# Kernel optimization log

Measured on AMD Instinct MI355X. Metric: run time of the kernel, lower is better.

The kernel has to match this reference:

```python
import jax, jax.numpy as jnp
import numpy as np

L, B, D = 1024, 24, 512


def setup_inputs() -> dict:
    key = jax.random.key(0)
    ks = jax.random.split(key, 9)
    s = 1.0 / np.sqrt(D)
    return {
        "v": jax.random.normal(ks[0], (L, B, D), dtype=jnp.float32),
        "h0": jax.random.normal(ks[1], (B, D), dtype=jnp.float32),
        "V": jax.random.normal(ks[2], (B, D), dtype=jnp.float32),
        "Wp": jax.random.normal(ks[3], (D, D), dtype=jnp.float32) * s,
        "Wp_": jax.random.normal(ks[4], (D, D), dtype=jnp.float32) * s,
        "w_ih": jax.random.normal(ks[5], (3 * D, D), dtype=jnp.float32) * s,
        "w_hh": jax.random.normal(ks[6], (3 * D, D), dtype=jnp.float32) * s,
        "b_ih": jax.random.normal(ks[7], (3 * D,), dtype=jnp.float32) * s,
        "b_hh": jax.random.normal(ks[8], (3 * D,), dtype=jnp.float32) * s,
    }


def reference(v, h0, V, Wp, Wp_, w_ih, w_hh, b_ih, b_hh):
    # v: [l, b, d]. Precompute both projections once (original wastefully
    # recomputes Wp_(v) per step; the math is identical).
    Wpv_all = jnp.einsum('lbd,hd->lbh', v, Wp)    # per-step query proj
    Wpvp = jnp.einsum('lbd,hd->lbh', v, Wp_)      # shared key proj

    def step(h, wpv_i):
        # additive attention over all l positions
        x = jnp.tanh(wpv_i[None, :, :] + Wpvp)           # [l, b, h]
        s = jnp.einsum('lbh,bh->bl', x, V)               # scores
        a = jax.nn.softmax(s, axis=1)                    # [b, l]
        c = jnp.einsum('bl,lbd->bd', a, v)               # context [b, d]
        # torch.nn.GRUCell math
        gi = c @ w_ih.T + b_ih
        gh = h @ w_hh.T + b_hh
        i_r, i_z, i_n = jnp.split(gi, 3, axis=1)
        h_r, h_z, h_n = jnp.split(gh, 3, axis=1)
        r = jax.nn.sigmoid(i_r + h_r)
        z = jax.nn.sigmoid(i_z + h_z)
        n = jnp.tanh(i_n + r * h_n)
        h_new = (1.0 - z) * n + z * h
        return h_new, h_new

    _, hs = jax.lax.scan(step, h0, Wpv_all)              # hs: [l, b, d]
    # dropout is identity in eval mode
    return hs
```

## Files before the change

### kernel.cpp

```cpp
#include <hip/hip_runtime.h>
#include <math.h>


__launch_bounds__(256, 2)
__global__ void gemm_abt_kernel(const float* __restrict__ A, const float* __restrict__ B,
                                float* __restrict__ out, int K, int N,
                                const float* __restrict__ bias, int do_tanh) {
  __shared__ __align__(16) float As[16][136];
  __shared__ __align__(16) float Bs[16][136];
  const int m0 = blockIdx.y * 128, n0 = blockIdx.x * 128;
  const int tid = threadIdx.x;
  const int tm = (tid & 15) * 8, tn = (tid >> 4) * 8;
  const int srow = tid & 127, scol = (tid >> 7) * 8;
  const float* Ap = A + (size_t)(m0 + srow) * K + scol;
  const float* Bp = B + (size_t)(n0 + srow) * K + scol;
  float acc[8][8] = {{0.f}};
  for (int k0 = 0; k0 < K; k0 += 16) {
    const float4 a0 = *(const float4*)(Ap + k0);
    const float4 a1 = *(const float4*)(Ap + k0 + 4);
    const float4 b0 = *(const float4*)(Bp + k0);
    const float4 b1 = *(const float4*)(Bp + k0 + 4);
    __syncthreads();
    As[scol + 0][srow] = a0.x; As[scol + 1][srow] = a0.y;
    As[scol + 2][srow] = a0.z; As[scol + 3][srow] = a0.w;
    As[scol + 4][srow] = a1.x; As[scol + 5][srow] = a1.y;
    As[scol + 6][srow] = a1.z; As[scol + 7][srow] = a1.w;
    Bs[scol + 0][srow] = b0.x; Bs[scol + 1][srow] = b0.y;
    Bs[scol + 2][srow] = b0.z; Bs[scol + 3][srow] = b0.w;
    Bs[scol + 4][srow] = b1.x; Bs[scol + 5][srow] = b1.y;
    Bs[scol + 6][srow] = b1.z; Bs[scol + 7][srow] = b1.w;
    __syncthreads();
#pragma unroll
    for (int kk = 0; kk < 16; ++kk) {
      const float4 av0 = *(const float4*)&As[kk][tm];
      const float4 av1 = *(const float4*)&As[kk][tm + 4];
      const float4 bv0 = *(const float4*)&Bs[kk][tn];
      const float4 bv1 = *(const float4*)&Bs[kk][tn + 4];
      const float ar[8] = {av0.x, av0.y, av0.z, av0.w, av1.x, av1.y, av1.z, av1.w};
      const float br[8] = {bv0.x, bv0.y, bv0.z, bv0.w, bv1.x, bv1.y, bv1.z, bv1.w};
#pragma unroll
      for (int r = 0; r < 8; ++r)
#pragma unroll
        for (int c = 0; c < 8; ++c)
          acc[r][c] = fmaf(ar[r], br[c], acc[r][c]);
    }
  }
#pragma unroll
  for (int r = 0; r < 8; ++r) {
    float* o = out + (size_t)(m0 + tm + r) * N + n0 + tn;
#pragma unroll
    for (int c = 0; c < 8; ++c) {
      float val = acc[r][c];
      if (bias) val += bias[n0 + tn + c];
      if (do_tanh) val = tanhf(val);
      o[c] = val;
    }
  }
}

__launch_bounds__(256, 3)
__global__ void attn_kernel(const float* __restrict__ tq, const float* __restrict__ tk,
                            const float* __restrict__ Vv, const float* __restrict__ v,
                            float* __restrict__ Cout) {
  const int b = blockIdx.y;
  const int it = blockIdx.x;
  const int tid = threadIdx.x;
  const int wave = tid >> 6, lane = tid & 63;
  const int h8 = lane * 8;
  __shared__ __align__(16) float sm[4][1024];
  __shared__ __align__(16) float red[4][4][512];
  __shared__ float inv_s[4];

  float q[4][8], vp[4][8];
  {
    const float* vvp = Vv + (size_t)b * 512 + h8;
    const float4 v0 = *(const float4*)vvp;
    const float4 v1 = *(const float4*)(vvp + 4);
    const float vv[8] = {v0.x, v0.y, v0.z, v0.w, v1.x, v1.y, v1.z, v1.w};
#pragma unroll
    for (int ii = 0; ii < 4; ++ii) {
      const float* qp = tq + ((size_t)(it * 4 + ii) * 24 + b) * 512 + h8;
      const float4 q0 = *(const float4*)qp;
      const float4 q1 = *(const float4*)(qp + 4);
      q[ii][0] = q0.x; q[ii][1] = q0.y; q[ii][2] = q0.z; q[ii][3] = q0.w;
      q[ii][4] = q1.x; q[ii][5] = q1.y; q[ii][6] = q1.z; q[ii][7] = q1.w;
#pragma unroll
      for (int j = 0; j < 8; ++j)
        vp[ii][j] = vv[j] * (1.0f - q[ii][j] * q[ii][j]);
    }
  }

  for (int l = wave; l < 1024; l += 4) {
    const float* kp = tk + ((size_t)l * 24 + b) * 512 + h8;
    const float4 k0 = *(const float4*)kp;
    const float4 k1 = *(const float4*)(kp + 4);
    const float kkv[8] = {k0.x, k0.y, k0.z, k0.w, k1.x, k1.y, k1.z, k1.w};
    float acc0 = 0.f, acc1 = 0.f, acc2 = 0.f, acc3 = 0.f;
#pragma unroll
    for (int j = 0; j < 8; ++j) {
      const float w = kkv[j];
      acc0 = fmaf(vp[0][j] * w, __builtin_amdgcn_rcpf(fmaf(q[0][j], w, 1.0f)), acc0);
      acc1 = fmaf(vp[1][j] * w, __builtin_amdgcn_rcpf(fmaf(q[1][j], w, 1.0f)), acc1);
      acc2 = fmaf(vp[2][j] * w, __builtin_amdgcn_rcpf(fmaf(q[2][j], w, 1.0f)), acc2);
      acc3 = fmaf(vp[3][j] * w, __builtin_amdgcn_rcpf(fmaf(q[3][j], w, 1.0f)), acc3);
    }
#pragma unroll
    for (int mask = 32; mask; mask >>= 1) {
      acc0 += __shfl_xor(acc0, mask, 64);
      acc1 += __shfl_xor(acc1, mask, 64);
      acc2 += __shfl_xor(acc2, mask, 64);
      acc3 += __shfl_xor(acc3, mask, 64);
    }
    if (lane == 0) {
      sm[0][l] = acc0; sm[1][l] = acc1; sm[2][l] = acc2; sm[3][l] = acc3;
    }
  }
  __syncthreads();

  {
    float* row = sm[wave];
    float m = -1e30f;
    for (int t = lane; t < 1024; t += 64) m = fmaxf(m, row[t]);
#pragma unroll
    for (int mask = 32; mask; mask >>= 1) m = fmaxf(m, __shfl_xor(m, mask, 64));
    float s = 0.f;
    for (int t = lane; t < 1024; t += 64) {
      const float e = __expf(row[t] - m);
      row[t] = e;
      s += e;
    }
#pragma unroll
    for (int mask = 32; mask; mask >>= 1) s += __shfl_xor(s, mask, 64);
    if (lane == 0) inv_s[wave] = 1.0f / s;
  }
  __syncthreads();

  float ca[4][8] = {{0.f}};
  const int l0 = wave * 256;
  for (int l = l0; l < l0 + 256; ++l) {
    const float* vrow = v + ((size_t)l * 24 + b) * 512 + h8;
    const float4 x0 = *(const float4*)vrow;
    const float4 x1 = *(const float4*)(vrow + 4);
    const float a0 = sm[0][l], a1 = sm[1][l], a2 = sm[2][l], a3 = sm[3][l];
    const float xv[8] = {x0.x, x0.y, x0.z, x0.w, x1.x, x1.y, x1.z, x1.w};
#pragma unroll
    for (int j = 0; j < 8; ++j) {
      ca[0][j] = fmaf(a0, xv[j], ca[0][j]);
      ca[1][j] = fmaf(a1, xv[j], ca[1][j]);
      ca[2][j] = fmaf(a2, xv[j], ca[2][j]);
      ca[3][j] = fmaf(a3, xv[j], ca[3][j]);
    }
  }
#pragma unroll
  for (int ii = 0; ii < 4; ++ii) {
    *(float4*)&red[wave][ii][h8]     = make_float4(ca[ii][0], ca[ii][1], ca[ii][2], ca[ii][3]);
    *(float4*)&red[wave][ii][h8 + 4] = make_float4(ca[ii][4], ca[ii][5], ca[ii][6], ca[ii][7]);
  }
  __syncthreads();
  {
    const int ii = tid >> 6;
    const int d0 = (tid & 63) * 8;
    float4 s0 = *(const float4*)&red[0][ii][d0];
    float4 s1 = *(const float4*)&red[0][ii][d0 + 4];
#pragma unroll
    for (int w = 1; w < 4; ++w) {
      const float4 r0 = *(const float4*)&red[w][ii][d0];
      const float4 r1 = *(const float4*)&red[w][ii][d0 + 4];
      s0.x += r0.x; s0.y += r0.y; s0.z += r0.z; s0.w += r0.w;
      s1.x += r1.x; s1.y += r1.y; s1.z += r1.z; s1.w += r1.w;
    }
    const float inv = inv_s[ii];
    s0.x *= inv; s0.y *= inv; s0.z *= inv; s0.w *= inv;
    s1.x *= inv; s1.y *= inv; s1.z *= inv; s1.w *= inv;
    float* o = Cout + ((size_t)(it * 4 + ii) * 24 + b) * 512 + d0;
    *(float4*)o = s0;
    *(float4*)(o + 4) = s1;
  }
}

union HPack {
  unsigned long long u;
  struct { float f; unsigned tag; } s;
};

__launch_bounds__(1024, 1)
__global__ void gru_persist_kernel(const float* __restrict__ Gi_c,
                                   const float* __restrict__ w_hh,
                                   const float* __restrict__ b_hh,
                                   const float* __restrict__ h0,
                                   unsigned long long* __restrict__ hb0,
                                   unsigned long long* __restrict__ hb1,
                                   float* __restrict__ out, int gstep0) {
  const int g  = blockIdx.x & 7;
  const int sl = blockIdx.x >> 3;
  const int t  = threadIdx.x;
  const int r  = t >> 5;
  const int kc = t & 31;
  const int dgr = sl * 32 + r;
  const bool pub = (kc == 0);

  __shared__ __align__(16) float h_lds[2][640];

  float wreg[3][16];
#pragma unroll
  for (int gg = 0; gg < 3; ++gg) {
    const float* wr = w_hh + (size_t)(gg * 512 + dgr) * 512 + kc * 16;
#pragma unroll
    for (int j = 0; j < 16; j += 4) {
      const float4 wv = *(const float4*)(wr + j);
      wreg[gg][j] = wv.x; wreg[gg][j + 1] = wv.y;
      wreg[gg][j + 2] = wv.z; wreg[gg][j + 3] = wv.w;
    }
  }
  const float bias_r = b_hh[dgr];
  const float bias_z = b_hh[512 + dgr];
  const float bias_n = b_hh[1024 + dgr];

  if (gstep0 == 0 && t < 96) {
    const int q = t >> 5, d = t & 31;
    const int bg = g * 3 + q;
    HPack p;
    p.s.f = h0[(size_t)bg * 512 + sl * 32 + d];
    p.s.tag = 1u;
    __hip_atomic_store(hb1 + (size_t)bg * 512 + sl * 32 + d, p.u,
                       __ATOMIC_RELAXED, __HIP_MEMORY_SCOPE_AGENT);
  }

  float hq[3];
  HPack pf;
  if (t < 512)
    pf.u = __hip_atomic_load(((gstep0 & 1) ? hb0 : hb1) + (size_t)(g * 3) * 512 + t,
                             __ATOMIC_RELAXED, __HIP_MEMORY_SCOPE_AGENT);

  for (int il = 0; il < 128; ++il) {
    const int gs = gstep0 + il;
#pragma unroll
    for (int q = 0; q < 3; ++q) {
      const int bg = g * 3 + q;
      const unsigned want = (unsigned)(gs + 1);
      const int buf = (il + q) & 1;

      if (t < 512) {
        const unsigned long long* src = ((gs & 1) ? hb0 : hb1) + (size_t)bg * 512 + t;
        HPack p = pf;
        {
          const int gs_n = (q == 2) ? gs + 1 : gs;
          const int bg_n = (q == 2) ? g * 3 : bg + 1;
          pf.u = __hip_atomic_load(((gs_n & 1) ? hb0 : hb1) + (size_t)bg_n * 512 + t,
                                   __ATOMIC_RELAXED, __HIP_MEMORY_SCOPE_AGENT);
        }
        while (p.s.tag < want) {
          p.u = __hip_atomic_load(src, __ATOMIC_RELAXED, __HIP_MEMORY_SCOPE_AGENT);
          if (p.s.tag >= want) break;
          __builtin_amdgcn_s_sleep(1);
        }
        h_lds[buf][t + ((t >> 4) << 2)] = p.s.f;
      }
      float gir = 0.f, giz = 0.f, gin = 0.f;
      if (pub) {
        const float* gi = Gi_c + ((size_t)il * 24 + bg) * 1536 + dgr;
        gir = gi[0]; giz = gi[512]; gin = gi[1024];
      }
      __syncthreads();
      if (il == 0 && pub) hq[q] = h_lds[buf][dgr + ((dgr >> 4) << 2)];

      const float* hbp = &h_lds[buf][kc * 20];
      float hv[16];
#pragma unroll
      for (int j = 0; j < 16; j += 4) {
        const float4 x = *(const float4*)(hbp + j);
        hv[j] = x.x; hv[j + 1] = x.y; hv[j + 2] = x.z; hv[j + 3] = x.w;
      }
      float sr = 0.f, sz = 0.f, sn = 0.f;
#pragma unroll
      for (int j = 0; j < 16; ++j) {
        sr = fmaf(hv[j], wreg[0][j], sr);
        sz = fmaf(hv[j], wreg[1][j], sz);
        sn = fmaf(hv[j], wreg[2][j], sn);
      }
#pragma unroll
      for (int mask = 1; mask <= 16; mask <<= 1) {
        sr += __shfl_xor(sr, mask, 64);
        sz += __shfl_xor(sz, mask, 64);
        sn += __shfl_xor(sn, mask, 64);
      }

      if (pub) {
        const float rg = __builtin_amdgcn_rcpf(1.0f + __expf(-(gir + sr + bias_r)));
        const float zg = __builtin_amdgcn_rcpf(1.0f + __expf(-(giz + sz + bias_z)));
        const float nx = gin + rg * (sn + bias_n);
        const float e2 = __expf(-2.0f * fabsf(nx));
        const float tn = __builtin_copysignf((1.0f - e2) * __builtin_amdgcn_rcpf(1.0f + e2), nx);
        const float hn = (1.0f - zg) * tn + zg * hq[q];
        hq[q] = hn;
        HPack pw; pw.s.f = hn; pw.s.tag = (unsigned)(gs + 2);
        __hip_atomic_store(((gs & 1) ? hb1 : hb0) + (size_t)bg * 512 + dgr, pw.u,
                           __ATOMIC_RELAXED, __HIP_MEMORY_SCOPE_AGENT);
        out[((size_t)gs * 24 + bg) * 512 + dgr] = hn;
      }
    }
  }
}

extern "C" void kernel_launch(void* const* d_in, const int* in_sizes, int n_in,
                              void* d_out, int out_size, void* d_ws, size_t ws_size,
                              hipStream_t stream) {
  (void)in_sizes; (void)n_in; (void)out_size;
  const float* v    = (const float*)d_in[0];
  const float* h0   = (const float*)d_in[1];
  const float* Vv   = (const float*)d_in[2];
  const float* Wp   = (const float*)d_in[3];
  const float* Wp_  = (const float*)d_in[4];
  const float* w_ih = (const float*)d_in[5];
  const float* w_hh = (const float*)d_in[6];
  const float* b_ih = (const float*)d_in[7];
  const float* b_hh = (const float*)d_in[8];
  float* out = (float*)d_out;

  const bool full_tq = ws_size >= (size_t)126025728;
  float* ws   = (float*)d_ws;
  float* tk   = ws;
  float* tqF  = tk + (size_t)12582912;
  float* tq_c = tk + (size_t)12582912;
  float* C_c  = full_tq ? (tqF + (size_t)12582912) : (tq_c + (size_t)1572864);
  float* Gi_c = C_c + (size_t)1572864;
  unsigned long long* hb0 = (unsigned long long*)(Gi_c + (size_t)4718592);
  unsigned long long* hb1 = hb0 + (size_t)12288;

  hipMemsetAsync(hb0, 0, (size_t)2 * 12288 * sizeof(unsigned long long), stream);

  gemm_abt_kernel<<<dim3(4, 192), 256, 0, stream>>>(v, Wp_, tk, 512, 512, nullptr, 1);
  if (full_tq)
    gemm_abt_kernel<<<dim3(4, 192), 256, 0, stream>>>(v, Wp, tqF, 512, 512, nullptr, 1);

  for (int c = 0; c < 8; ++c) {
    const float* v_chunk = v + (size_t)c * 128 * 24 * 512;
    const float* tq_use;
    if (full_tq) {
      tq_use = tqF + (size_t)c * 128 * 24 * 512;
    } else {
      gemm_abt_kernel<<<dim3(4, 24), 256, 0, stream>>>(v_chunk, Wp, tq_c, 512, 512, nullptr, 1);
      tq_use = tq_c;
    }
    attn_kernel<<<dim3(32, 24), 256, 0, stream>>>(tq_use, tk, Vv, v, C_c);
    gemm_abt_kernel<<<dim3(12, 24), 256, 0, stream>>>(C_c, w_ih, Gi_c, 512, 1536, b_ih, 0);
    gru_persist_kernel<<<128, 1024, 0, stream>>>(Gi_c, w_hh, b_hh, h0, hb0, hb1,
                                                 out, c * 128);
  }
}
```

Before: 8.852 ms.

## Spread GRU recurrence over 256 blocks, batch three sequences per sync

The persistent GRU kernel now runs on 256 blocks, each owning 16 hidden rows instead of 32. The w_hh slice is staged in LDS rather than held in registers. All three batch rows of a group are fetched and synchronised together once per timestep instead of three separate fetch/sync/reduce rounds. Each wave computes nine dot products with a full 64-lane shuffle reduction. The aim is to cut per-step barriers and serial latency on the recurrent critical path, at the cost of more blocks that must be co-resident for the spin-wait protocol and more LDS traffic.

```diff
diff --git a/kernel.cpp b/kernel.cpp
--- a/kernel.cpp
+++ b/kernel.cpp
@@ -194,110 +194,131 @@
   const int g  = blockIdx.x & 7;
   const int sl = blockIdx.x >> 3;
   const int t  = threadIdx.x;
-  const int r  = t >> 5;
-  const int kc = t & 31;
-  const int dgr = sl * 32 + r;
-  const bool pub = (kc == 0);
-
-  __shared__ __align__(16) float h_lds[2][640];
-
-  float wreg[3][16];
-#pragma unroll
-  for (int gg = 0; gg < 3; ++gg) {
-    const float* wr = w_hh + (size_t)(gg * 512 + dgr) * 512 + kc * 16;
-#pragma unroll
-    for (int j = 0; j < 16; j += 4) {
-      const float4 wv = *(const float4*)(wr + j);
-      wreg[gg][j] = wv.x; wreg[gg][j + 1] = wv.y;
-      wreg[gg][j + 2] = wv.z; wreg[gg][j + 3] = wv.w;
-    }
+  const int w  = t >> 6;
+  const int l  = t & 63;
+  const int dgr = sl * 16 + w;
+
+  __shared__ __align__(16) float w_lds[48][576];
+  __shared__ __align__(16) float h_stage[2][3][576];
+
+  for (int e = t; e < 24576; e += 1024) {
+    const int k = e & 511, gr = e >> 9;
+    const int gg = gr >> 4, r = gr & 15;
+    w_lds[gr][k + ((k >> 5) << 2)] =
+        w_hh[(size_t)(gg * 512 + sl * 16 + r) * 512 + k];
   }
   const float bias_r = b_hh[dgr];
   const float bias_z = b_hh[512 + dgr];
   const float bias_n = b_hh[1024 + dgr];
 
-  if (gstep0 == 0 && t < 96) {
-    const int q = t >> 5, d = t & 31;
+  if (gstep0 == 0 && t < 48) {
+    const int q = t >> 4, d = t & 15;
     const int bg = g * 3 + q;
-    HPack p;
-    p.s.f = h0[(size_t)bg * 512 + sl * 32 + d];
-    p.s.tag = 1u;
-    __hip_atomic_store(hb1 + (size_t)bg * 512 + sl * 32 + d, p.u,
+    HPack p; p.s.f = h0[(size_t)bg * 512 + sl * 16 + d]; p.s.tag = 1u;
+    __hip_atomic_store(hb1 + (size_t)bg * 512 + sl * 16 + d, p.u,
                        __ATOMIC_RELAXED, __HIP_MEMORY_SCOPE_AGENT);
   }
 
-  float hq[3];
-  HPack pf;
-  if (t < 512)
-    pf.u = __hip_atomic_load(((gstep0 & 1) ? hb0 : hb1) + (size_t)(g * 3) * 512 + t,
-                             __ATOMIC_RELAXED, __HIP_MEMORY_SCOPE_AGENT);
+  const int d0 = t & 511;
+  const int q0 = t >> 9;
+  const bool two = (t < 512);
+
+  float hq = 0.f;
 
   for (int il = 0; il < 128; ++il) {
     const int gs = gstep0 + il;
-#pragma unroll
-    for (int q = 0; q < 3; ++q) {
-      const int bg = g * 3 + q;
-      const unsigned want = (unsigned)(gs + 1);
-      const int buf = (il + q) & 1;
-
-      if (t < 512) {
-        const unsigned long long* src = ((gs & 1) ? hb0 : hb1) + (size_t)bg * 512 + t;
-        HPack p = pf;
-        {
-          const int gs_n = (q == 2) ? gs + 1 : gs;
-          const int bg_n = (q == 2) ? g * 3 : bg + 1;
-          pf.u = __hip_atomic_load(((gs_n & 1) ? hb0 : hb1) + (size_t)bg_n * 512 + t,
-                                   __ATOMIC_RELAXED, __HIP_MEMORY_SCOPE_AGENT);
-        }
-        while (p.s.tag < want) {
-          p.u = __hip_atomic_load(src, __ATOMIC_RELAXED, __HIP_MEMORY_SCOPE_AGENT);
-          if (p.s.tag >= want) break;
-          __builtin_amdgcn_s_sleep(1);
-        }
-        h_lds[buf][t + ((t >> 4) << 2)] = p.s.f;
+    const unsigned want = (unsigned)(gs + 1);
+    const unsigned long long* hbR = (gs & 1) ? hb0 : hb1;
+    unsigned long long* hbW = (gs & 1) ? hb1 : hb0;
+    const int buf = il & 1;
+
+    float gir = 0.f, giz = 0.f, gin = 0.f;
+    if (l < 3) {
+      const float* gi = Gi_c + ((size_t)il * 24 + (g * 3 + l)) * 1536 + dgr;
+      gir = gi[0]; giz = gi[512]; gin = gi[1024];
+    }
+
+    {
+      const unsigned long long* s1 = hbR + (size_t)(g * 3 + q0) * 512 + d0;
+      const unsigned long long* s2 = hbR + (size_t)(g * 3 + 2) * 512 + d0;
+      HPack p1, p2;
+      p1.u = __hip_atomic_load(s1, __ATOMIC_RELAXED, __HIP_MEMORY_SCOPE_AGENT);
+      p2.u = two ? __hip_atomic_load(s2, __ATOMIC_RELAXED, __HIP_MEMORY_SCOPE_AGENT)
+                 : p1.u;
+      while (p1.s.tag < want || p2.s.tag < want) {
+        __builtin_amdgcn_s_sleep(1);
+        if (p1.s.tag < want)
+          p1.u = __hip_atomic_load(s1, __ATOMIC_RELAXED, __HIP_MEMORY_SCOPE_AGENT);
+        if (p2.s.tag < want)
+          p2.u = two ? __hip_atomic_load(s2, __ATOMIC_RELAXED, __HIP_MEMORY_SCOPE_AGENT)
+                     : p1.u;
       }
-      float gir = 0.f, giz = 0.f, gin = 0.f;
-      if (pub) {
-        const float* gi = Gi_c + ((size_t)il * 24 + bg) * 1536 + dgr;
-        gir = gi[0]; giz = gi[512]; gin = gi[1024];
-      }
-      __syncthreads();
-      if (il == 0 && pub) hq[q] = h_lds[buf][dgr + ((dgr >> 4) << 2)];
-
-      const float* hbp = &h_lds[buf][kc * 20];
-      float hv[16];
-#pragma unroll
-      for (int j = 0; j < 16; j += 4) {
-        const float4 x = *(const float4*)(hbp + j);
-        hv[j] = x.x; hv[j + 1] = x.y; hv[j + 2] = x.z; hv[j + 3] = x.w;
-      }
-      float sr = 0.f, sz = 0.f, sn = 0.f;
-#pragma unroll
-      for (int j = 0; j < 16; ++j) {
-        sr = fmaf(hv[j], wreg[0][j], sr);
-        sz = fmaf(hv[j], wreg[1][j], sz);
-        sn = fmaf(hv[j], wreg[2][j], sn);
-      }
-#pragma unroll
-      for (int mask = 1; mask <= 16; mask <<= 1) {
-        sr += __shfl_xor(sr, mask, 64);
-        sz += __shfl_xor(sz, mask, 64);
-        sn += __shfl_xor(sn, mask, 64);
-      }
-
-      if (pub) {
-        const float rg = __builtin_amdgcn_rcpf(1.0f + __expf(-(gir + sr + bias_r)));
-        const float zg = __builtin_amdgcn_rcpf(1.0f + __expf(-(giz + sz + bias_z)));
-        const float nx = gin + rg * (sn + bias_n);
-        const float e2 = __expf(-2.0f * fabsf(nx));
-        const float tn = __builtin_copysignf((1.0f - e2) * __builtin_amdgcn_rcpf(1.0f + e2), nx);
-        const float hn = (1.0f - zg) * tn + zg * hq[q];
-        hq[q] = hn;
-        HPack pw; pw.s.f = hn; pw.s.tag = (unsigned)(gs + 2);
-        __hip_atomic_store(((gs & 1) ? hb1 : hb0) + (size_t)bg * 512 + dgr, pw.u,
-                           __ATOMIC_RELAXED, __HIP_MEMORY_SCOPE_AGENT);
-        out[((size_t)gs * 24 + bg) * 512 + dgr] = hn;
-      }
+      const int sk = d0 + ((d0 >> 5) << 2);
+      h_stage[buf][q0][sk] = p1.s.f;
+      if (two) h_stage[buf][2][sk] = p2.s.f;
+    }
+    __syncthreads();
+    if (il == 0 && l < 3) hq = h_stage[buf][l][dgr + ((dgr >> 5) << 2)];
+
+    const int base = (l << 3) + ((l >> 2) << 2);
+    const float4 wA0 = *(const float4*)&w_lds[w][base];
+    const float4 wA1 = *(const float4*)&w_lds[w][base + 4];
+    const float4 wB0 = *(const float4*)&w_lds[16 + w][base];
+    const float4 wB1 = *(const float4*)&w_lds[16 + w][base + 4];
+    const float4 wC0 = *(const float4*)&w_lds[32 + w][base];
+    const float4 wC1 = *(const float4*)&w_lds[32 + w][base + 4];
+    const float4 hA0 = *(const float4*)&h_stage[buf][0][base];
+    const float4 hA1 = *(const float4*)&h_stage[buf][0][base + 4];
+    const float4 hB0 = *(const float4*)&h_stage[buf][1][base];
+    const float4 hB1 = *(const float4*)&h_stage[buf][1][base + 4];
+    const float4 hC0 = *(const float4*)&h_stage[buf][2][base];
+    const float4 hC1 = *(const float4*)&h_stage[buf][2][base + 4];
+
+#define DOT8(W0, W1, X0, X1)                                                  \
+  fmaf((W1).w, (X1).w, fmaf((W1).z, (X1).z, fmaf((W1).y, (X1).y,              \
+  fmaf((W1).x, (X1).x, fmaf((W0).w, (X0).w, fmaf((W0).z, (X0).z,              \
+  fmaf((W0).y, (X0).y, (W0).x * (X0).x)))))))
+
+    float sAr = DOT8(wA0, wA1, hA0, hA1);
+    float sAz = DOT8(wB0, wB1, hA0, hA1);
+    float sAn = DOT8(wC0, wC1, hA0, hA1);
+    float sBr = DOT8(wA0, wA1, hB0, hB1);
+    float sBz = DOT8(wB0, wB1, hB0, hB1);
+    float sBn = DOT8(wC0, wC1, hB0, hB1);
+    float sCr = DOT8(wA0, wA1, hC0, hC1);
+    float sCz = DOT8(wB0, wB1, hC0, hC1);
+    float sCn = DOT8(wC0, wC1, hC0, hC1);
+#undef DOT8
+
+#pragma unroll
+    for (int m = 1; m < 64; m <<= 1) {
+      sAr += __shfl_xor(sAr, m, 64);
+      sAz += __shfl_xor(sAz, m, 64);
+      sAn += __shfl_xor(sAn, m, 64);
+      sBr += __shfl_xor(sBr, m, 64);
+      sBz += __shfl_xor(sBz, m, 64);
+      sBn += __shfl_xor(sBn, m, 64);
+      sCr += __shfl_xor(sCr, m, 64);
+      sCz += __shfl_xor(sCz, m, 64);
+      sCn += __shfl_xor(sCn, m, 64);
+    }
+
+    if (l < 3) {
+      const int bg = g * 3 + l;
+      const float sr = (l == 0) ? sAr : (l == 1) ? sBr : sCr;
+      const float sz = (l == 0) ? sAz : (l == 1) ? sBz : sCz;
+      const float sn = (l == 0) ? sAn : (l == 1) ? sBn : sCn;
+      const float rg = __builtin_amdgcn_rcpf(1.0f + __expf(-(gir + sr + bias_r)));
+      const float zg = __builtin_amdgcn_rcpf(1.0f + __expf(-(giz + sz + bias_z)));
+      const float nx = gin + rg * (sn + bias_n);
+      const float e2 = __expf(-2.0f * fabsf(nx));
+      const float tn = __builtin_copysignf((1.0f - e2) * __builtin_amdgcn_rcpf(1.0f + e2), nx);
+      const float hn = (1.0f - zg) * tn + zg * hq;
+      hq = hn;
+      HPack pw; pw.s.f = hn; pw.s.tag = (unsigned)(gs + 2);
+      __hip_atomic_store(hbW + (size_t)bg * 512 + dgr, pw.u,
+                         __ATOMIC_RELAXED, __HIP_MEMORY_SCOPE_AGENT);
+      out[((size_t)gs * 24 + bg) * 512 + dgr] = hn;
     }
   }
 }
@@ -344,7 +365,7 @@
     }
     attn_kernel<<<dim3(32, 24), 256, 0, stream>>>(tq_use, tk, Vv, v, C_c);
     gemm_abt_kernel<<<dim3(12, 24), 256, 0, stream>>>(C_c, w_ih, Gi_c, 512, 1536, b_ih, 0);
-    gru_persist_kernel<<<128, 1024, 0, stream>>>(Gi_c, w_hh, b_hh, h0, hb0, hb1,
+    gru_persist_kernel<<<256, 1024, 0, stream>>>(Gi_c, w_hh, b_hh, h0, hb0, hb1,
                                                  out, c * 128);
   }
 }
```

Measured after the change: 13.46 ms. +52.1%, slower.

## Split GRU recurrence over 256 blocks with w_hh in LDS and wave-wide reductions

Applied to the files above, without the earlier changes.

The persistent GRU kernel now runs on 256 blocks, each owning 16 hidden rows instead of 32. The block's w_hh slice moves from registers into padded LDS, and each wave reduces a full 512-length dot product across 64 lanes. The change also prefetches two batches ahead, hoists the Gi loads out of the per-batch loop, and lengthens the spin sleep. The intent is to spread the serial recurrence over more CUs so each step does less work. In exchange, more producers and consumers take part in the global tag handshake, every step reads weights from LDS, and the shuffle reduction gets longer.

```diff
diff --git a/kernel.cpp b/kernel.cpp
--- a/kernel.cpp
+++ b/kernel.cpp
@@ -194,107 +194,120 @@
   const int g  = blockIdx.x & 7;
   const int sl = blockIdx.x >> 3;
   const int t  = threadIdx.x;
-  const int r  = t >> 5;
-  const int kc = t & 31;
-  const int dgr = sl * 32 + r;
-  const bool pub = (kc == 0);
-
-  __shared__ __align__(16) float h_lds[2][640];
-
-  float wreg[3][16];
-#pragma unroll
-  for (int gg = 0; gg < 3; ++gg) {
-    const float* wr = w_hh + (size_t)(gg * 512 + dgr) * 512 + kc * 16;
-#pragma unroll
-    for (int j = 0; j < 16; j += 4) {
-      const float4 wv = *(const float4*)(wr + j);
-      wreg[gg][j] = wv.x; wreg[gg][j + 1] = wv.y;
-      wreg[gg][j + 2] = wv.z; wreg[gg][j + 3] = wv.w;
-    }
+  const int w  = t >> 6;
+  const int l  = t & 63;
+  const int dgr = sl * 16 + w;
+
+  __shared__ __align__(16) float w_lds[48][576];
+  __shared__ __align__(16) float h_stage[2][576];
+
+  for (int e = t; e < 24576; e += 1024) {
+    const int k = e & 511, gr = e >> 9;
+    const int gg = gr >> 4, r = gr & 15;
+    w_lds[gr][k + ((k >> 5) << 2)] =
+        w_hh[(size_t)(gg * 512 + sl * 16 + r) * 512 + k];
   }
   const float bias_r = b_hh[dgr];
   const float bias_z = b_hh[512 + dgr];
   const float bias_n = b_hh[1024 + dgr];
 
-  if (gstep0 == 0 && t < 96) {
-    const int q = t >> 5, d = t & 31;
+  if (gstep0 == 0 && t < 48) {
+    const int q = t >> 4, d = t & 15;
     const int bg = g * 3 + q;
-    HPack p;
-    p.s.f = h0[(size_t)bg * 512 + sl * 32 + d];
-    p.s.tag = 1u;
-    __hip_atomic_store(hb1 + (size_t)bg * 512 + sl * 32 + d, p.u,
+    HPack p; p.s.f = h0[(size_t)bg * 512 + sl * 16 + d]; p.s.tag = 1u;
+    __hip_atomic_store(hb1 + (size_t)bg * 512 + sl * 16 + d, p.u,
                        __ATOMIC_RELAXED, __HIP_MEMORY_SCOPE_AGENT);
   }
 
   float hq[3];
-  HPack pf;
-  if (t < 512)
-    pf.u = __hip_atomic_load(((gstep0 & 1) ? hb0 : hb1) + (size_t)(g * 3) * 512 + t,
-                             __ATOMIC_RELAXED, __HIP_MEMORY_SCOPE_AGENT);
+  HPack pf0, pf1;
+  {
+    const unsigned long long* hbR0 = (gstep0 & 1) ? hb0 : hb1;
+    if (t < 512) {
+      pf0.u = __hip_atomic_load(hbR0 + (size_t)(g * 3 + 0) * 512 + t,
+                                __ATOMIC_RELAXED, __HIP_MEMORY_SCOPE_AGENT);
+      pf1.u = __hip_atomic_load(hbR0 + (size_t)(g * 3 + 1) * 512 + t,
+                                __ATOMIC_RELAXED, __HIP_MEMORY_SCOPE_AGENT);
+    }
+  }
 
   for (int il = 0; il < 128; ++il) {
     const int gs = gstep0 + il;
+    const unsigned want = (unsigned)(gs + 1);
+    const unsigned long long* hbR = (gs & 1) ? hb0 : hb1;
+    unsigned long long* hbW = (gs & 1) ? hb1 : hb0;
+
+    float gir[3], giz[3], gin[3];
+    if (l == 0) {
+      const float* gi = Gi_c + ((size_t)il * 24 + g * 3) * 1536 + dgr;
+#pragma unroll
+      for (int q = 0; q < 3; ++q) {
+        gir[q] = gi[q * 1536];
+        giz[q] = gi[q * 1536 + 512];
+        gin[q] = gi[q * 1536 + 1024];
+      }
+    }
+
 #pragma unroll
     for (int q = 0; q < 3; ++q) {
       const int bg = g * 3 + q;
-      const unsigned want = (unsigned)(gs + 1);
       const int buf = (il + q) & 1;
 
       if (t < 512) {
-        const unsigned long long* src = ((gs & 1) ? hb0 : hb1) + (size_t)bg * 512 + t;
-        HPack p = pf;
-        {
-          const int gs_n = (q == 2) ? gs + 1 : gs;
-          const int bg_n = (q == 2) ? g * 3 : bg + 1;
-          pf.u = __hip_atomic_load(((gs_n & 1) ? hb0 : hb1) + (size_t)bg_n * 512 + t,
-                                   __ATOMIC_RELAXED, __HIP_MEMORY_SCOPE_AGENT);
-        }
+        HPack p = pf0;
+        pf0 = pf1;
+        const unsigned long long* nsrc =
+            (q == 0) ? hbR + ((size_t)(g * 3 + 2) * 512 + t)
+          : (q == 1) ? hbW + ((size_t)(g * 3 + 0) * 512 + t)
+                     : hbW + ((size_t)(g * 3 + 1) * 512 + t);
+        pf1.u = __hip_atomic_load(nsrc, __ATOMIC_RELAXED, __HIP_MEMORY_SCOPE_AGENT);
+        const unsigned long long* src = hbR + (size_t)bg * 512 + t;
         while (p.s.tag < want) {
           p.u = __hip_atomic_load(src, __ATOMIC_RELAXED, __HIP_MEMORY_SCOPE_AGENT);
           if (p.s.tag >= want) break;
-          __builtin_amdgcn_s_sleep(1);
+          __builtin_amdgcn_s_sleep(2);
         }
-        h_lds[buf][t + ((t >> 4) << 2)] = p.s.f;
-      }
-      float gir = 0.f, giz = 0.f, gin = 0.f;
-      if (pub) {
-        const float* gi = Gi_c + ((size_t)il * 24 + bg) * 1536 + dgr;
-        gir = gi[0]; giz = gi[512]; gin = gi[1024];
+        h_stage[buf][t + ((t >> 5) << 2)] = p.s.f;
       }
       __syncthreads();
-      if (il == 0 && pub) hq[q] = h_lds[buf][dgr + ((dgr >> 4) << 2)];
-
-      const float* hbp = &h_lds[buf][kc * 20];
-      float hv[16];
-#pragma unroll
-      for (int j = 0; j < 16; j += 4) {
-        const float4 x = *(const float4*)(hbp + j);
-        hv[j] = x.x; hv[j + 1] = x.y; hv[j + 2] = x.z; hv[j + 3] = x.w;
+      if (il == 0 && l == 0) hq[q] = h_stage[buf][dgr + ((dgr >> 5) << 2)];
+
+      const int base = (l << 3) + ((l >> 2) << 2);
+      const float4 wR0 = *(const float4*)&w_lds[w][base];
+      const float4 wR1 = *(const float4*)&w_lds[w][base + 4];
+      const float4 wZ0 = *(const float4*)&w_lds[16 + w][base];
+      const float4 wZ1 = *(const float4*)&w_lds[16 + w][base + 4];
+      const float4 wN0 = *(const float4*)&w_lds[32 + w][base];
+      const float4 wN1 = *(const float4*)&w_lds[32 + w][base + 4];
+      const float4 hh0 = *(const float4*)&h_stage[buf][base];
+      const float4 hh1 = *(const float4*)&h_stage[buf][base + 4];
+
+#define DOT8(W0, W1, X0, X1)                                                  \
+  fmaf((W1).w, (X1).w, fmaf((W1).z, (X1).z, fmaf((W1).y, (X1).y,              \
+  fmaf((W1).x, (X1).x, fmaf((W0).w, (X0).w, fmaf((W0).z, (X0).z,              \
+  fmaf((W0).y, (X0).y, (W0).x * (X0).x)))))))
+      float sr = DOT8(wR0, wR1, hh0, hh1);
+      float sz = DOT8(wZ0, wZ1, hh0, hh1);
+      float sn = DOT8(wN0, wN1, hh0, hh1);
+#undef DOT8
+
+#pragma unroll
+      for (int m = 1; m < 64; m <<= 1) {
+        sr += __shfl_xor(sr, m, 64);
+        sz += __shfl_xor(sz, m, 64);
+        sn += __shfl_xor(sn, m, 64);
       }
-      float sr = 0.f, sz = 0.f, sn = 0.f;
-#pragma unroll
-      for (int j = 0; j < 16; ++j) {
-        sr = fmaf(hv[j], wreg[0][j], sr);
-        sz = fmaf(hv[j], wreg[1][j], sz);
-        sn = fmaf(hv[j], wreg[2][j], sn);
-      }
-#pragma unroll
-      for (int mask = 1; mask <= 16; mask <<= 1) {
-        sr += __shfl_xor(sr, mask, 64);
-        sz += __shfl_xor(sz, mask, 64);
-        sn += __shfl_xor(sn, mask, 64);
-      }
-
-      if (pub) {
-        const float rg = __builtin_amdgcn_rcpf(1.0f + __expf(-(gir + sr + bias_r)));
-        const float zg = __builtin_amdgcn_rcpf(1.0f + __expf(-(giz + sz + bias_z)));
-        const float nx = gin + rg * (sn + bias_n);
+
+      if (l == 0) {
+        const float rg = __builtin_amdgcn_rcpf(1.0f + __expf(-(gir[q] + sr + bias_r)));
+        const float zg = __builtin_amdgcn_rcpf(1.0f + __expf(-(giz[q] + sz + bias_z)));
+        const float nx = gin[q] + rg * (sn + bias_n);
         const float e2 = __expf(-2.0f * fabsf(nx));
         const float tn = __builtin_copysignf((1.0f - e2) * __builtin_amdgcn_rcpf(1.0f + e2), nx);
         const float hn = (1.0f - zg) * tn + zg * hq[q];
         hq[q] = hn;
         HPack pw; pw.s.f = hn; pw.s.tag = (unsigned)(gs + 2);
-        __hip_atomic_store(((gs & 1) ? hb1 : hb0) + (size_t)bg * 512 + dgr, pw.u,
+        __hip_atomic_store(hbW + (size_t)bg * 512 + dgr, pw.u,
                            __ATOMIC_RELAXED, __HIP_MEMORY_SCOPE_AGENT);
         out[((size_t)gs * 24 + bg) * 512 + dgr] = hn;
       }
@@ -344,7 +357,7 @@
     }
     attn_kernel<<<dim3(32, 24), 256, 0, stream>>>(tq_use, tk, Vv, v, C_c);
     gemm_abt_kernel<<<dim3(12, 24), 256, 0, stream>>>(C_c, w_ih, Gi_c, 512, 1536, b_ih, 0);
-    gru_persist_kernel<<<128, 1024, 0, stream>>>(Gi_c, w_hh, b_hh, h0, hb0, hb1,
+    gru_persist_kernel<<<256, 1024, 0, stream>>>(Gi_c, w_hh, b_hh, h0, hb0, hb1,
                                                  out, c * 128);
   }
 }
```

Result: slower. 10.94 ms (+23.6%).

## Restructure persistent GRU kernel to process two batch rows per sync with 512 threads

Applied to the files above, without the earlier changes.

The persistent GRU recurrence kernel now uses 512-thread blocks, with each block covering 16 hidden rows across 6 batch rows in a group of 4, instead of 32 rows across 3 batch rows in a group of 8. Each sub-step handles two batch rows at once, so the same w_hh values are reused for two h vectors, and the K reduction is split across quarters and combined through a small LDS buffer. Weights are reread from global/L2 each step instead of being held in registers. The goal is fewer cross-block spin-wait rounds per step and more arithmetic per wait. The cost is an extra __syncthreads per sub-step and weight traffic from memory on every step.

```diff
diff --git a/kernel.cpp b/kernel.cpp
--- a/kernel.cpp
+++ b/kernel.cpp
@@ -183,7 +183,7 @@
   struct { float f; unsigned tag; } s;
 };
 
-__launch_bounds__(1024, 1)
+__launch_bounds__(512, 1)
 __global__ void gru_persist_kernel(const float* __restrict__ Gi_c,
                                    const float* __restrict__ w_hh,
                                    const float* __restrict__ b_hh,
@@ -191,112 +191,155 @@
                                    unsigned long long* __restrict__ hb0,
                                    unsigned long long* __restrict__ hb1,
                                    float* __restrict__ out, int gstep0) {
-  const int g  = blockIdx.x & 7;
-  const int sl = blockIdx.x >> 3;
+  const int g  = blockIdx.x & 3;
+  const int sl = blockIdx.x >> 2;
   const int t  = threadIdx.x;
-  const int r  = t >> 5;
-  const int kc = t & 31;
-  const int dgr = sl * 32 + r;
-  const bool pub = (kc == 0);
-
-  __shared__ __align__(16) float h_lds[2][640];
-
-  float wreg[3][16];
-#pragma unroll
-  for (int gg = 0; gg < 3; ++gg) {
-    const float* wr = w_hh + (size_t)(gg * 512 + dgr) * 512 + kc * 16;
-#pragma unroll
-    for (int j = 0; j < 16; j += 4) {
-      const float4 wv = *(const float4*)(wr + j);
-      wreg[gg][j] = wv.x; wreg[gg][j + 1] = wv.y;
-      wreg[gg][j + 2] = wv.z; wreg[gg][j + 3] = wv.w;
-    }
-  }
-  const float bias_r = b_hh[dgr];
-  const float bias_z = b_hh[512 + dgr];
-  const float bias_n = b_hh[1024 + dgr];
+  const int w  = t >> 6;
+  const int l  = t & 63;
+  const int og = l >> 3;
+  const int kc = l & 7;
+  const int row = ((w & 1) << 3) + og;
+  const int quarter = w >> 1;
+  const int dgr = sl * 16 + row;
+
+  __shared__ __align__(16) float h_lds[2][2][640];
+  __shared__ float red[2][3][16][5];
 
   if (gstep0 == 0 && t < 96) {
-    const int q = t >> 5, d = t & 31;
-    const int bg = g * 3 + q;
-    HPack p;
-    p.s.f = h0[(size_t)bg * 512 + sl * 32 + d];
-    p.s.tag = 1u;
-    __hip_atomic_store(hb1 + (size_t)bg * 512 + sl * 32 + d, p.u,
+    const int q = t >> 4, d = t & 15;
+    const int bg = g * 6 + q;
+    HPack p; p.s.f = h0[(size_t)bg * 512 + sl * 16 + d]; p.s.tag = 1u;
+    __hip_atomic_store(hb1 + (size_t)bg * 512 + sl * 16 + d, p.u,
                        __ATOMIC_RELAXED, __HIP_MEMORY_SCOPE_AGENT);
   }
 
+  const int prow = t >> 1, pb = t & 1;
+  const int pdgr = sl * 16 + prow;
+  float pbias_r = 0.f, pbias_z = 0.f, pbias_n = 0.f;
+  if (t < 32) {
+    pbias_r = b_hh[pdgr]; pbias_z = b_hh[512 + pdgr]; pbias_n = b_hh[1024 + pdgr];
+  }
+
+  const float* wr_p = w_hh + ((size_t)dgr          << 9) + quarter * 128 + kc * 16;
+  const float* wz_p = w_hh + ((size_t)(512 + dgr)  << 9) + quarter * 128 + kc * 16;
+  const float* wn_p = w_hh + ((size_t)(1024 + dgr) << 9) + quarter * 128 + kc * 16;
+
   float hq[3];
-  HPack pf;
-  if (t < 512)
-    pf.u = __hip_atomic_load(((gstep0 & 1) ? hb0 : hb1) + (size_t)(g * 3) * 512 + t,
-                             __ATOMIC_RELAXED, __HIP_MEMORY_SCOPE_AGENT);
+
+  HPack pfA0, pfB0, pfA1, pfB1;
+  {
+    const unsigned long long* hbR0 = (gstep0 & 1) ? hb0 : hb1;
+    pfA0.u = __hip_atomic_load(hbR0 + (size_t)(g * 6 + 0) * 512 + t,
+                               __ATOMIC_RELAXED, __HIP_MEMORY_SCOPE_AGENT);
+    pfB0.u = __hip_atomic_load(hbR0 + (size_t)(g * 6 + 1) * 512 + t,
+                               __ATOMIC_RELAXED, __HIP_MEMORY_SCOPE_AGENT);
+    pfA1.u = __hip_atomic_load(hbR0 + (size_t)(g * 6 + 2) * 512 + t,
+                               __ATOMIC_RELAXED, __HIP_MEMORY_SCOPE_AGENT);
+    pfB1.u = __hip_atomic_load(hbR0 + (size_t)(g * 6 + 3) * 512 + t,
+                               __ATOMIC_RELAXED, __HIP_MEMORY_SCOPE_AGENT);
+  }
 
   for (int il = 0; il < 128; ++il) {
     const int gs = gstep0 + il;
-#pragma unroll
-    for (int q = 0; q < 3; ++q) {
-      const int bg = g * 3 + q;
-      const unsigned want = (unsigned)(gs + 1);
-      const int buf = (il + q) & 1;
-
-      if (t < 512) {
-        const unsigned long long* src = ((gs & 1) ? hb0 : hb1) + (size_t)bg * 512 + t;
-        HPack p = pf;
-        {
-          const int gs_n = (q == 2) ? gs + 1 : gs;
-          const int bg_n = (q == 2) ? g * 3 : bg + 1;
-          pf.u = __hip_atomic_load(((gs_n & 1) ? hb0 : hb1) + (size_t)bg_n * 512 + t,
+    const unsigned want = (unsigned)(gs + 1);
+    const unsigned long long* hbR = (gs & 1) ? hb0 : hb1;
+    unsigned long long* hbW = (gs & 1) ? hb1 : hb0;
+
+#pragma unroll
+    for (int s = 0; s < 3; ++s) {
+      const int bgA = g * 6 + 2 * s;
+      const int buf = (il + s) & 1;
+
+      float gir = 0.f, giz = 0.f, gin = 0.f;
+      if (t < 32) {
+        const float* gi = Gi_c + ((size_t)il * 24 + bgA + pb) * 1536 + pdgr;
+        gir = gi[0]; giz = gi[512]; gin = gi[1024];
+      }
+
+      HPack pA = pfA0, pB = pfB0;
+      pfA0 = pfA1; pfB0 = pfB1;
+      {
+        const int ns  = (s + 2) % 3;
+        const int ngs = gs + (s >= 1 ? 1 : 0);
+        const unsigned long long* hbR2 = (ngs & 1) ? hb0 : hb1;
+        pfA1.u = __hip_atomic_load(hbR2 + (size_t)(g * 6 + 2 * ns) * 512 + t,
                                    __ATOMIC_RELAXED, __HIP_MEMORY_SCOPE_AGENT);
-        }
-        while (p.s.tag < want) {
-          p.u = __hip_atomic_load(src, __ATOMIC_RELAXED, __HIP_MEMORY_SCOPE_AGENT);
-          if (p.s.tag >= want) break;
-          __builtin_amdgcn_s_sleep(1);
-        }
-        h_lds[buf][t + ((t >> 4) << 2)] = p.s.f;
-      }
-      float gir = 0.f, giz = 0.f, gin = 0.f;
-      if (pub) {
-        const float* gi = Gi_c + ((size_t)il * 24 + bg) * 1536 + dgr;
-        gir = gi[0]; giz = gi[512]; gin = gi[1024];
-      }
+        pfB1.u = __hip_atomic_load(hbR2 + (size_t)(g * 6 + 2 * ns + 1) * 512 + t,
+                                   __ATOMIC_RELAXED, __HIP_MEMORY_SCOPE_AGENT);
+      }
+      const unsigned long long* srcA = hbR + (size_t)bgA * 512 + t;
+      const unsigned long long* srcB = srcA + 512;
+      while (pA.s.tag < want) {
+        pA.u = __hip_atomic_load(srcA, __ATOMIC_RELAXED, __HIP_MEMORY_SCOPE_AGENT);
+        if (pA.s.tag >= want) break;
+        __builtin_amdgcn_s_sleep(2);
+      }
+      while (pB.s.tag < want) {
+        pB.u = __hip_atomic_load(srcB, __ATOMIC_RELAXED, __HIP_MEMORY_SCOPE_AGENT);
+        if (pB.s.tag >= want) break;
+        __builtin_amdgcn_s_sleep(2);
+      }
+      const int sk = ((t >> 4) * 20) + (t & 15);
+      h_lds[buf][0][sk] = pA.s.f;
+      h_lds[buf][1][sk] = pB.s.f;
       __syncthreads();
-      if (il == 0 && pub) hq[q] = h_lds[buf][dgr + ((dgr >> 4) << 2)];
-
-      const float* hbp = &h_lds[buf][kc * 20];
-      float hv[16];
+      if (il == 0 && t < 32)
+        hq[s] = h_lds[buf][pb][((pdgr & 511) >> 4) * 20 + (pdgr & 15)];
+
+      const float* hA = &h_lds[buf][0][(quarter * 8 + kc) * 20];
+      const float* hB = &h_lds[buf][1][(quarter * 8 + kc) * 20];
+      float sAr = 0.f, sAz = 0.f, sAn = 0.f, sBr = 0.f, sBz = 0.f, sBn = 0.f;
 #pragma unroll
       for (int j = 0; j < 16; j += 4) {
-        const float4 x = *(const float4*)(hbp + j);
-        hv[j] = x.x; hv[j + 1] = x.y; hv[j + 2] = x.z; hv[j + 3] = x.w;
-      }
-      float sr = 0.f, sz = 0.f, sn = 0.f;
-#pragma unroll
-      for (int j = 0; j < 16; ++j) {
-        sr = fmaf(hv[j], wreg[0][j], sr);
-        sz = fmaf(hv[j], wreg[1][j], sz);
-        sn = fmaf(hv[j], wreg[2][j], sn);
-      }
-#pragma unroll
-      for (int mask = 1; mask <= 16; mask <<= 1) {
-        sr += __shfl_xor(sr, mask, 64);
-        sz += __shfl_xor(sz, mask, 64);
-        sn += __shfl_xor(sn, mask, 64);
-      }
-
-      if (pub) {
-        const float rg = __builtin_amdgcn_rcpf(1.0f + __expf(-(gir + sr + bias_r)));
-        const float zg = __builtin_amdgcn_rcpf(1.0f + __expf(-(giz + sz + bias_z)));
-        const float nx = gin + rg * (sn + bias_n);
+        const float4 wr = *(const float4*)(wr_p + j);
+        const float4 wz = *(const float4*)(wz_p + j);
+        const float4 wn = *(const float4*)(wn_p + j);
+        const float4 ha = *(const float4*)(hA + j);
+        const float4 hb = *(const float4*)(hB + j);
+        sAr = fmaf(wr.x, ha.x, fmaf(wr.y, ha.y, fmaf(wr.z, ha.z, fmaf(wr.w, ha.w, sAr))));
+        sBr = fmaf(wr.x, hb.x, fmaf(wr.y, hb.y, fmaf(wr.z, hb.z, fmaf(wr.w, hb.w, sBr))));
+        sAz = fmaf(wz.x, ha.x, fmaf(wz.y, ha.y, fmaf(wz.z, ha.z, fmaf(wz.w, ha.w, sAz))));
+        sBz = fmaf(wz.x, hb.x, fmaf(wz.y, hb.y, fmaf(wz.z, hb.z, fmaf(wz.w, hb.w, sBz))));
+        sAn = fmaf(wn.x, ha.x, fmaf(wn.y, ha.y, fmaf(wn.z, ha.z, fmaf(wn.w, ha.w, sAn))));
+        sBn = fmaf(wn.x, hb.x, fmaf(wn.y, hb.y, fmaf(wn.z, hb.z, fmaf(wn.w, hb.w, sBn))));
+      }
+#pragma unroll
+      for (int m = 1; m <= 4; m <<= 1) {
+        sAr += __shfl_xor(sAr, m, 64);
+        sAz += __shfl_xor(sAz, m, 64);
+        sAn += __shfl_xor(sAn, m, 64);
+        sBr += __shfl_xor(sBr, m, 64);
+        sBz += __shfl_xor(sBz, m, 64);
+        sBn += __shfl_xor(sBn, m, 64);
+      }
+      if (kc == 0) {
+        red[0][0][row][quarter] = sAr;
+        red[0][1][row][quarter] = sAz;
+        red[0][2][row][quarter] = sAn;
+        red[1][0][row][quarter] = sBr;
+        red[1][1][row][quarter] = sBz;
+        red[1][2][row][quarter] = sBn;
+      }
+      __syncthreads();
+
+      if (t < 32) {
+        const float* r0 = red[pb][0][prow];
+        const float* r1 = red[pb][1][prow];
+        const float* r2 = red[pb][2][prow];
+        const float sr = (r0[0] + r0[1]) + (r0[2] + r0[3]);
+        const float sz = (r1[0] + r1[1]) + (r1[2] + r1[3]);
+        const float sn = (r2[0] + r2[1]) + (r2[2] + r2[3]);
+        const float rg = __builtin_amdgcn_rcpf(1.0f + __expf(-(gir + sr + pbias_r)));
+        const float zg = __builtin_amdgcn_rcpf(1.0f + __expf(-(giz + sz + pbias_z)));
+        const float nx = gin + rg * (sn + pbias_n);
         const float e2 = __expf(-2.0f * fabsf(nx));
         const float tn = __builtin_copysignf((1.0f - e2) * __builtin_amdgcn_rcpf(1.0f + e2), nx);
-        const float hn = (1.0f - zg) * tn + zg * hq[q];
-        hq[q] = hn;
+        const float hn = (1.0f - zg) * tn + zg * hq[s];
+        hq[s] = hn;
         HPack pw; pw.s.f = hn; pw.s.tag = (unsigned)(gs + 2);
-        __hip_atomic_store(((gs & 1) ? hb1 : hb0) + (size_t)bg * 512 + dgr, pw.u,
+        __hip_atomic_store(hbW + (size_t)(bgA + pb) * 512 + pdgr, pw.u,
                            __ATOMIC_RELAXED, __HIP_MEMORY_SCOPE_AGENT);
-        out[((size_t)gs * 24 + bg) * 512 + dgr] = hn;
+        out[((size_t)gs * 24 + bgA + pb) * 512 + pdgr] = hn;
       }
     }
   }
@@ -344,7 +387,7 @@
     }
     attn_kernel<<<dim3(32, 24), 256, 0, stream>>>(tq_use, tk, Vv, v, C_c);
     gemm_abt_kernel<<<dim3(12, 24), 256, 0, stream>>>(C_c, w_ih, Gi_c, 512, 1536, b_ih, 0);
-    gru_persist_kernel<<<128, 1024, 0, stream>>>(Gi_c, w_hh, b_hh, h0, hb0, hb1,
-                                                 out, c * 128);
+    gru_persist_kernel<<<128, 512, 0, stream>>>(Gi_c, w_hh, b_hh, h0, hb0, hb1,
+                                                out, c * 128);
   }
 }
```

Measured after the change: 9.165 ms. 3.5% more time.
